# Kernel tuning notes

Hardware: AMD Instinct MI355X
Metric: run time of the kernel (lower is better)

The kernel has to match this reference:

```python
import jax, jax.numpy as jnp
import numpy as np

V, H, L, A, TH, B, T = 32000, 512, 4, 384, 2, 2, 32
FF = 4 * H


def _ln(x, w, b, eps=1e-5):
    m = x.mean(-1, keepdims=True)
    v = ((x - m) ** 2).mean(-1, keepdims=True)
    return (x - m) * jax.lax.rsqrt(v + eps) * w + b


def setup_inputs() -> dict:
    key = jax.random.key(0)
    ks = jax.random.split(key, 10)
    w = lambda k, shape, s=0.02: jax.random.normal(k, shape, jnp.float32) * s
    return {
        "input_ids": jax.random.randint(ks[0], (B, T), 0, V),
        "states": w(ks[1], (L, B, H, H), 0.1),
        "emb": w(ks[2], (V, H)),
        "nx_w": jnp.ones((L, H)), "nx_b": jnp.zeros((L, H)),
        "Wp": w(ks[3], (L, A + H, H)), "bp": jnp.zeros((L, A + H)),
        "Wg": w(ks[4], (L, H, H)), "Wt": w(ks[5], (L, H, H)),
        "ns_w": jnp.ones((L, H)), "ns_b": jnp.zeros((L, H)),
        "W1": w(ks[6], (L, FF, H)), "b1": jnp.zeros((L, FF)),
        "W2": w(ks[7], (L, H, FF)), "b2": jnp.zeros((L, H)),
        "on_w": jnp.ones((H,)), "on_b": jnp.zeros((H,)),
        "head_W": w(ks[8], (V, H)), "head_b": jnp.zeros((V,)),
    }


def _recur(lp, state, x):
    # state: [B,H,H]; x: [B,H]. Rank-1 low-rank update of the active rows,
    # gated tanh update of the ghost rows (Finch/Goose + GhostRNN).
    p = x @ lp["Wp"].T + lp["bp"]                  # [B, A+H]
    u, v = p[:, :A], p[:, A:]
    active_upd = u[:, :, None] * v[:, None, :]       # [B,A,H] = u @ v (rank 1)
    ghost = state[:, A:]                             # [B,H-A,H]
    gate = jax.nn.sigmoid(jnp.einsum('bgh,oh->bgo', ghost, lp["Wg"]))
    trans = jnp.tanh(jnp.einsum('bgh,oh->bgo', ghost, lp["Wt"]))
    return state + jnp.concatenate([active_upd, gate * trans], axis=1)


def _layer(lp, state, x):
    state = _recur(lp, state, _ln(x, lp["nx_w"], lp["nx_b"]))
    z = jnp.zeros_like(x)
    for _ in range(TH - 1):                          # latent "thinking" steps
        state = _recur(lp, state, z)
    x = x + state.mean(axis=1)                       # [B,H]
    h = _ln(x, lp["ns_w"], lp["ns_b"])
    h = jax.nn.gelu(h @ lp["W1"].T + lp["b1"], approximate=False)
    return state, x + h @ lp["W2"].T + lp["b2"]


def _forward(input_ids, states, emb, nx_w, nx_b, Wp, bp, Wg, Wt, ns_w, ns_b,
             W1, b1, W2, b2, on_w, on_b, head_W, head_b):
    lp = dict(nx_w=nx_w, nx_b=nx_b, Wp=Wp, bp=bp, Wg=Wg, Wt=Wt,
              ns_w=ns_w, ns_b=ns_b, W1=W1, b1=b1, W2=W2, b2=b2)
    x = jnp.swapaxes(emb[input_ids], 0, 1)           # [T,B,H]

    def step(st, tok):                               # scan over time
        def lstep(tok, inp):                         # scan over layers
            lpi, s = inp
            s, tok = _layer(lpi, s, tok)
            return tok, s
        tok, new_st = jax.lax.scan(lstep, tok, (lp, st))
        return new_st, tok

    fstates, outs = jax.lax.scan(step, states, x)    # outs: [T,B,H]
    y = _ln(jnp.swapaxes(outs, 0, 1), on_w, on_b)
    return y @ head_W.T + head_b, fstates


def reference(input_ids, states, emb, nx_w, nx_b, Wp, bp, Wg, Wt, ns_w, ns_b,
              W1, b1, W2, b2, on_w, on_b, head_W, head_b):
    return _forward(input_ids, states, emb, nx_w, nx_b, Wp, bp, Wg, Wt,
                    ns_w, ns_b, W1, b1, W2, b2, on_w, on_b, head_W, head_b)
```

## Files before the change

kernel.cpp:

```cpp
#include <hip/hip_runtime.h>
#include <hip/hip_bf16.h>
#include <math.h>
#include <stddef.h>

namespace {

constexpr int V = 32000, H = 512, L = 4, A = 384, B = 2, T = 32, FF = 2048;
constexpr long LOGITS = (long)B * T * V;
constexpr int GRID = 256, NT = 512;
constexpr int NXR = 32;
constexpr int NGB = 32;
constexpr float EPS = 1e-5f;

typedef short bf16x8 __attribute__((ext_vector_type(8)));
typedef float f32x4 __attribute__((ext_vector_type(4)));
typedef unsigned long long ull;
typedef unsigned long long ull2 __attribute__((ext_vector_type(2)));

struct WS {
  unsigned gbar_cnt, gbar_gen;
  unsigned pad0[62];
  unsigned p1c[L], p2c[L], p3c[L], grc[L];
  unsigned pad1[48];
  unsigned gcol_cnt2[L][T];
  unsigned gxcnt[L];
  unsigned gxcd[L][NGB];
  unsigned pad2[64];
  float gcol[L][T][B][H];
  float uv[T][L][B][A + H];
  float lnxs[T][L][B][H];
  float outs[T][B][H];
  float lnouts[T * B][H];
  float xn[3][T][B][H];
  float hbuf[L][2][B][FF];
  float initcol[L * B * H];
  float bus[4];
  float wU[L][H];
  uint4 bpk[L][2][2][16][32][64];
  ull afr[L][2][2][2][8][16][64][2];
};

union __align__(16) SMem {
  struct { unsigned xch[8][2][16][16]; float colp[8][2][16]; } gx;
  struct {
    unsigned wp[16][256];
    unsigned w1[64][256];
    unsigned w2[16][1024];
    float lnx[2][512];
    unsigned hb[2][1024];
    float xms[2][16];
    float2 red[8];
  } xp;
  struct { float u16[T][16]; float lnx[H]; } e1;
  struct { float tile[125][64]; } hd;
};

__device__ __forceinline__ float dot4(const float4& a, const float4& b) {
  return a.x * b.x + a.y * b.y + a.z * b.z + a.w * b.w;
}
__device__ __forceinline__ unsigned bf16r(float f) {
  unsigned u = __float_as_uint(f);
  return (u + 0x7fffu + ((u >> 16) & 1u)) >> 16;
}
__device__ __forceinline__ float sload(const float* p) {
  return __hip_atomic_load(p, __ATOMIC_RELAXED, __HIP_MEMORY_SCOPE_SYSTEM);
}
__device__ __forceinline__ void sstore(float* p, float v) {
  __hip_atomic_store(p, v, __ATOMIC_RELAXED, __HIP_MEMORY_SCOPE_SYSTEM);
}
__device__ __forceinline__ ull sld64(const ull* p) {
  return __hip_atomic_load(p, __ATOMIC_RELAXED, __HIP_MEMORY_SCOPE_SYSTEM);
}
__device__ __forceinline__ void sst64(ull* p, ull v) {
  __hip_atomic_store(p, v, __ATOMIC_RELAXED, __HIP_MEMORY_SCOPE_SYSTEM);
}
__device__ __forceinline__ ull ald64(const ull* p) {
  return __hip_atomic_load(p, __ATOMIC_RELAXED, __HIP_MEMORY_SCOPE_AGENT);
}
__device__ __forceinline__ void ast64(ull* p, ull v) {
  __hip_atomic_store(p, v, __ATOMIC_RELAXED, __HIP_MEMORY_SCOPE_AGENT);
}
__device__ __forceinline__ unsigned sload_u(const unsigned* p) {
  return __hip_atomic_load(p, __ATOMIC_RELAXED, __HIP_MEMORY_SCOPE_SYSTEM);
}
__device__ __forceinline__ f32x4 mfma16(bf16x8 a, bf16x8 b, f32x4 c) {
  return __builtin_amdgcn_mfma_f32_16x16x32_bf16(a, b, c, 0, 0, 0);
}
__device__ __forceinline__ bf16x8 bc2(ull a, ull b) {
  ull2 t; t.x = a; t.y = b;
  return __builtin_bit_cast(bf16x8, t);
}
__device__ __forceinline__ bf16x8 bcu4(uint4 u) {
  return __builtin_bit_cast(bf16x8, u);
}

template <bool FAST>
__device__ __forceinline__ bf16x8 ld_afr(const ull* p) {
  if (FAST) return bc2(ald64(p), ald64(p + 1));
  else      return bc2(sld64(p), sld64(p + 1));
}
template <bool FAST>
__device__ __forceinline__ void st_afr(ull* p, ull lo, ull hi) {
  if (FAST) { ast64(p, lo); ast64(p + 1, hi); }
  else      { sst64(p, lo); sst64(p + 1, hi); }
}

__device__ void wait_u32(unsigned* p, unsigned target) {
  int spin = 0;
  while (__hip_atomic_load(p, __ATOMIC_RELAXED, __HIP_MEMORY_SCOPE_AGENT) < target) {
    __builtin_amdgcn_s_sleep(8);
    if ((++spin & 63) == 0)
      (void)__hip_atomic_load(p, __ATOMIC_ACQUIRE, __HIP_MEMORY_SCOPE_AGENT);
  }
}

__device__ void gbar(WS* ws) {
  __syncthreads();
  if (threadIdx.x == 0) {
    __threadfence();
    unsigned g = __hip_atomic_load(&ws->gbar_gen, __ATOMIC_RELAXED, __HIP_MEMORY_SCOPE_AGENT);
    unsigned a = __hip_atomic_fetch_add(&ws->gbar_cnt, 1u, __ATOMIC_ACQ_REL, __HIP_MEMORY_SCOPE_AGENT);
    if (a == (unsigned)(GRID - 1)) {
      __hip_atomic_store(&ws->gbar_cnt, 0u, __ATOMIC_RELAXED, __HIP_MEMORY_SCOPE_AGENT);
      __hip_atomic_fetch_add(&ws->gbar_gen, 1u, __ATOMIC_RELEASE, __HIP_MEMORY_SCOPE_AGENT);
    } else {
      wait_u32(&ws->gbar_gen, g + 1);
    }
    __threadfence();
  }
  __syncthreads();
}

__device__ void cdone(unsigned* p) {
  __builtin_amdgcn_s_waitcnt(0);
  __syncthreads();
  if (threadIdx.x == 0)
    __hip_atomic_fetch_add(p, 1u, __ATOMIC_RELAXED, __HIP_MEMORY_SCOPE_AGENT);
}
__device__ void cwait(unsigned* p, unsigned tgt) {
  if (threadIdx.x == 0) {
    int spin = 0;
    while (sload_u(p) < tgt) {
      __builtin_amdgcn_s_sleep(2);
      if ((++spin & 1023) == 0)
        (void)__hip_atomic_load(p, __ATOMIC_ACQUIRE, __HIP_MEMORY_SCOPE_AGENT);
    }
  }
  __syncthreads();
}
__device__ void cwait2(unsigned* pa, unsigned ta, unsigned* pb, unsigned tbv) {
  if (threadIdx.x < 64) {
    unsigned* p = pa;
    unsigned tg = ta;
    if (threadIdx.x == 1) { p = pb; tg = tbv; }
    const bool act = threadIdx.x < 2;
    int spin = 0;
    for (;;) {
      bool ok = !act || sload_u(p) >= tg;
      if (__all(ok)) break;
      __builtin_amdgcn_s_sleep(2);
      if ((++spin & 1023) == 0 && act)
        (void)__hip_atomic_load(p, __ATOMIC_ACQUIRE, __HIP_MEMORY_SCOPE_AGENT);
    }
  }
  __syncthreads();
}

__device__ float2 wred2(float2 v) {
  #pragma unroll
  for (int off = 1; off < 64; off <<= 1) {
    v.x += __shfl_xor(v.x, off);
    v.y += __shfl_xor(v.y, off);
  }
  return v;
}

__device__ float2 block_red2(float2 v, SMem& sm) {
  v = wred2(v);
  int w = threadIdx.x >> 6;
  __syncthreads();
  if ((threadIdx.x & 63) == 0) sm.xp.red[w] = v;
  __syncthreads();
  float2 s{0.f, 0.f};
  #pragma unroll
  for (int q = 0; q < 8; ++q) { s.x += sm.xp.red[q].x; s.y += sm.xp.red[q].y; }
  return s;
}

__device__ void ln512(SMem& sm, const float* in, float* outp,
                      const float* w, const float* b) {
  int tid = threadIdx.x;
  float xv = in[tid];
  float m = block_red2({xv, 0.f}, sm).x * (1.f / H);
  float d = xv - m;
  float var = block_red2({d * d, 0.f}, sm).x * (1.f / H);
  float inv = rsqrtf(var + EPS);
  outp[tid] = d * inv * w[tid] + b[tid];
  __syncthreads();
}

__device__ float2 ln2reg(SMem& sm, float x0, float x1, const float* w, const float* b) {
  int tid = threadIdx.x;
  float2 mm = block_red2({x0, x1}, sm);
  float d0 = x0 - mm.x * (1.f / H), d1 = x1 - mm.y * (1.f / H);
  float2 vv = block_red2({d0 * d0, d1 * d1}, sm);
  float i0 = rsqrtf(vv.x * (1.f / H) + EPS), i1 = rsqrtf(vv.y * (1.f / H) + EPS);
  float wv_ = w[tid], bv = b[tid];
  float l0 = d0 * i0 * wv_ + bv, l1 = d1 * i1 * wv_ + bv;
  sm.xp.lnx[0][tid] = l0;
  sm.xp.lnx[1][tid] = l1;
  __syncthreads();
  return {l0, l1};
}

__device__ __forceinline__ float2 d8(uint4 wq, const float* xr0, const float* xr1) {
  float2 a{0.f, 0.f};
  unsigned u[4] = {wq.x, wq.y, wq.z, wq.w};
  #pragma unroll
  for (int j = 0; j < 4; ++j) {
    float wl = __uint_as_float(u[j] << 16);
    float wh = __uint_as_float(u[j] & 0xffff0000u);
    a.x = fmaf(wl, xr0[2 * j], fmaf(wh, xr0[2 * j + 1], a.x));
    a.y = fmaf(wl, xr1[2 * j], fmaf(wh, xr1[2 * j + 1], a.y));
  }
  return a;
}

template <bool FAST>
__device__ void ghost_regs(int l, int ct, WS* ws, SMem& sm,
                           const float* __restrict__ states, float* __restrict__ fs) {
  const int tid = threadIdx.x, wv = tid >> 6, lane = tid & 63;
  const int c15 = lane & 15, lq = lane >> 4;
  float ms[2][4];
  #pragma unroll
  for (int b = 0; b < 2; ++b)
    #pragma unroll
    for (int r = 0; r < 4; ++r)
      ms[b][r] = states[((((long)l * B + b) * H) + A + 16 * wv + 4 * lq + r) * H + 16 * ct + c15];

  const int ktp = ct >> 1;
  const int lt_base = 32 * (ct & 1);

  #pragma unroll 1
  for (int rec = 0; rec < 2 * T; ++rec) {
    const int pp = rec & 1, np = pp ^ 1;
    asm volatile("" ::: "memory");
    f32x4 accg[2], acct[2];
    #pragma unroll
    for (int b = 0; b < 2; ++b) { accg[b] = {0.f,0.f,0.f,0.f}; acct[b] = {0.f,0.f,0.f,0.f}; }
    #pragma unroll 4
    for (int kt = 0; kt < 16; ++kt) {
      bf16x8 a00 = ld_afr<FAST>(&ws->afr[l][pp][0][0][wv][kt][lane][0]);
      bf16x8 a01 = ld_afr<FAST>(&ws->afr[l][pp][0][1][wv][kt][lane][0]);
      bf16x8 a10 = ld_afr<FAST>(&ws->afr[l][pp][1][0][wv][kt][lane][0]);
      bf16x8 a11 = ld_afr<FAST>(&ws->afr[l][pp][1][1][wv][kt][lane][0]);
      bf16x8 bgh = bcu4(ws->bpk[l][0][0][kt][ct][lane]);
      bf16x8 bgl = bcu4(ws->bpk[l][0][1][kt][ct][lane]);
      bf16x8 bth = bcu4(ws->bpk[l][1][0][kt][ct][lane]);
      bf16x8 btl = bcu4(ws->bpk[l][1][1][kt][ct][lane]);
      accg[0] = mfma16(a00, bgh, accg[0]);
      accg[0] = mfma16(a00, bgl, accg[0]);
      accg[0] = mfma16(a01, bgh, accg[0]);
      acct[0] = mfma16(a00, bth, acct[0]);
      acct[0] = mfma16(a00, btl, acct[0]);
      acct[0] = mfma16(a01, bth, acct[0]);
      accg[1] = mfma16(a10, bgh, accg[1]);
      accg[1] = mfma16(a10, bgl, accg[1]);
      accg[1] = mfma16(a11, bgh, accg[1]);
      acct[1] = mfma16(a10, bth, acct[1]);
      acct[1] = mfma16(a10, btl, acct[1]);
      acct[1] = mfma16(a11, bth, acct[1]);
    }
    const int t = rec >> 1;
    const bool pub = (rec & 1) != 0;
    #pragma unroll
    for (int b = 0; b < 2; ++b) {
      float css = 0.f;
      #pragma unroll
      for (int r = 0; r < 4; ++r) {
        float sig = 1.f / (1.f + expf(-accg[b][r]));
        float nv = ms[b][r] + sig * tanhf(acct[b][r]);
        ms[b][r] = nv;
        css += nv;
        unsigned hi = bf16r(nv);
        unsigned lo = bf16r(nv - __uint_as_float(hi << 16));
        sm.gx.xch[wv][b][4 * lq + r][c15] = hi | (lo << 16);
      }
      if (pub) {
        css += __shfl_xor(css, 16);
        css += __shfl_xor(css, 32);
        if (lane < 16) sm.gx.colp[wv][b][lane] = css;
      }
    }
    __syncthreads();
    {
      const int b = lane >> 5, o2 = (lane >> 4) & 1, row = lane & 15;
      unsigned x[8];
      #pragma unroll
      for (int j = 0; j < 8; ++j) x[j] = sm.gx.xch[wv][b][row][o2 * 8 + j];
      unsigned hw[4], lw[4];
      #pragma unroll
      for (int j = 0; j < 4; ++j) {
        hw[j] = (x[2 * j] & 0xffffu) | ((x[2 * j + 1] & 0xffffu) << 16);
        lw[j] = (x[2 * j] >> 16) | (x[2 * j + 1] & 0xffff0000u);
      }
      const int lt = lt_base + 16 * o2 + row;
      st_afr<FAST>(&ws->afr[l][np][b][0][wv][ktp][lt][0],
                   hw[0] | ((ull)hw[1] << 32), hw[2] | ((ull)hw[3] << 32));
      st_afr<FAST>(&ws->afr[l][np][b][1][wv][ktp][lt][0],
                   lw[0] | ((ull)lw[1] << 32), lw[2] | ((ull)lw[3] << 32));
    }
    if (pub && tid < 32) {
      int b = tid >> 4, c = tid & 15;
      float s = 0.f;
      #pragma unroll
      for (int w = 0; w < 8; ++w) s += sm.gx.colp[w][b][c];
      sstore(&ws->gcol[l][t][b][16 * ct + c], s);
    }
    asm volatile("" ::: "memory");
    __builtin_amdgcn_s_waitcnt(0);
    __syncthreads();
    if (tid == 0) {
      __hip_atomic_fetch_add(&ws->grc[l], 1u, __ATOMIC_RELAXED, __HIP_MEMORY_SCOPE_AGENT);
      if (pub)
        __hip_atomic_fetch_add(&ws->gcol_cnt2[l][t], 1u, __ATOMIC_RELAXED, __HIP_MEMORY_SCOPE_AGENT);
    }
    if (rec + 1 < 2 * T) cwait(&ws->grc[l], (unsigned)(NGB * (rec + 1)));
  }
  #pragma unroll
  for (int b = 0; b < 2; ++b)
    #pragma unroll
    for (int r = 0; r < 4; ++r)
      fs[((((long)l * B + b) * H) + A + 16 * wv + 4 * lq + r) * H + 16 * ct + c15] = ms[b][r];
}

__device__ void x_set(int l, int role, WS* ws, SMem& sm,
                      const int* ids, const float* emb,
                      const float* nx_w, const float* nx_b,
                      const float* Wp, const float* bp,
                      const float* ns_w, const float* ns_b,
                      const float* W1, const float* b1,
                      const float* W2, const float* b2) {
  const int tid = threadIdx.x, wv = tid >> 6, lane = tid & 63;
  const long wb = (long)l * (A + H);
  const int v0r = role * 16, a0 = role * 64, c0 = role * 16;

  for (int i = tid; i < 16 * 256; i += NT) {
    int row = i >> 8, m = i & 255;
    const float* s = Wp + (wb + A + v0r + row) * H + 2 * m;
    sm.xp.wp[row][m] = bf16r(s[0]) | (bf16r(s[1]) << 16);
  }
  for (int i = tid; i < 64 * 256; i += NT) {
    int row = i >> 8, m = i & 255;
    const float* s = W1 + ((long)l * FF + a0 + row) * H + 2 * m;
    sm.xp.w1[row][m] = bf16r(s[0]) | (bf16r(s[1]) << 16);
  }
  for (int i = tid; i < 16 * 1024; i += NT) {
    int row = i >> 10, m = i & 1023;
    const float* s = W2 + ((long)l * H + c0 + row) * FF + 2 * m;
    sm.xp.w2[row][m] = bf16r(s[0]) | (bf16r(s[1]) << 16);
  }
  const float ic0 = ws->initcol[(l * B + 0) * H + tid];
  const float ic1 = ws->initcol[(l * B + 1) * H + tid];
  const float BU = ws->bus[l];
  const float bpA = bp[wb + A + tid];
  const float wU0 = ws->wU[l][tid];
  float as0 = 0.f, as1 = 0.f;
  __syncthreads();

  for (int t = 0; t < T; ++t) {
    float xm0, xm1;
    if (l == 0) {
      xm0 = emb[(long)ids[t] * H + tid];
      xm1 = emb[(long)ids[T + t] * H + tid];
    } else {
      cwait(&ws->p3c[l - 1], (unsigned)(NXR * (t + 1)));
      xm0 = sload(&ws->xn[l - 1][t][0][tid]);
      xm1 = sload(&ws->xn[l - 1][t][1][tid]);
    }
    float2 ln = ln2reg(sm, xm0, xm1, nx_w + l * H, nx_b + l * H);
    float xr0[8], xr1[8];
    #pragma unroll
    for (int j = 0; j < 8; ++j) { xr0[j] = sm.xp.lnx[0][lane * 8 + j]; xr1[j] = sm.xp.lnx[1][lane * 8 + j]; }
    #pragma unroll
    for (int it = 0; it < 2; ++it) {
      int row = v0r + wv + it * 8;
      uint4 wq = *(const uint4*)&sm.xp.wp[row - v0r][lane * 4];
      float2 acc = wred2(d8(wq, xr0, xr1));
      if (lane == 0) {
        float bb = bp[wb + A + row];
        sstore(&ws->uv[t][l][0][A + row], acc.x + bb);
        sstore(&ws->uv[t][l][1][A + row], acc.y + bb);
      }
    }
    if (tid >= v0r && tid < v0r + 16) {
      sstore(&ws->lnxs[t][l][0][tid], ln.x);
      sstore(&ws->lnxs[t][l][1][tid], ln.y);
    }
    cdone(&ws->p1c[l]);
    float2 U1 = block_red2({wU0 * ln.x, wU0 * ln.y}, sm);
    cwait2(&ws->p1c[l], (unsigned)(NXR * (t + 1)),
           &ws->gcol_cnt2[l][t], (unsigned)NGB);
    float v0 = sload(&ws->uv[t][l][0][A + tid]);
    float v1 = sload(&ws->uv[t][l][1][A + tid]);
    float gc0 = sload(&ws->gcol[l][t][0][tid]);
    float gc1 = sload(&ws->gcol[l][t][1][tid]);
    as0 += (U1.x + BU) * v0;
    as1 += (U1.y + BU) * v1;
    float tb = (float)(t + 1) * BU * bpA;
    xm0 += (as0 + ic0 + tb + gc0) * (1.f / H);
    xm1 += (as1 + ic1 + tb + gc1) * (1.f / H);
    if (tid >= c0 && tid < c0 + 16) { sm.xp.xms[0][tid - c0] = xm0; sm.xp.xms[1][tid - c0] = xm1; }
    ln = ln2reg(sm, xm0, xm1, ns_w + l * H, ns_b + l * H);
    #pragma unroll
    for (int j = 0; j < 8; ++j) { xr0[j] = sm.xp.lnx[0][lane * 8 + j]; xr1[j] = sm.xp.lnx[1][lane * 8 + j]; }
    #pragma unroll
    for (int it = 0; it < 8; ++it) {
      int row = a0 + wv + it * 8;
      uint4 wq = *(const uint4*)&sm.xp.w1[row - a0][lane * 4];
      float2 acc = wred2(d8(wq, xr0, xr1));
      if (lane == 0) {
        float bb = b1[(long)l * FF + row];
        float z0 = acc.x + bb, z1 = acc.y + bb;
        sstore(&ws->hbuf[l][t & 1][0][row], 0.5f * z0 * (1.f + erff(z0 * 0.70710678118f)));
        sstore(&ws->hbuf[l][t & 1][1][row], 0.5f * z1 * (1.f + erff(z1 * 0.70710678118f)));
      }
    }
    cdone(&ws->p2c[l]);
    cwait(&ws->p2c[l], (unsigned)(NXR * (t + 1)));
    for (int i = tid; i < 2048; i += NT) {
      int b = i >> 10, m = i & 1023;
      float h0 = sload(&ws->hbuf[l][t & 1][b][2 * m]);
      float h1 = sload(&ws->hbuf[l][t & 1][b][2 * m + 1]);
      sm.xp.hb[b][m] = bf16r(h0) | (bf16r(h1) << 16);
    }
    __syncthreads();
    unsigned h0r[16], h1r[16];
    #pragma unroll
    for (int q = 0; q < 16; ++q) { h0r[q] = sm.xp.hb[0][lane + 64 * q]; h1r[q] = sm.xp.hb[1][lane + 64 * q]; }
    #pragma unroll
    for (int it = 0; it < 2; ++it) {
      int row = c0 + wv + it * 8;
      float2 acc{0.f, 0.f};
      #pragma unroll
      for (int q = 0; q < 16; ++q) {
        unsigned w = sm.xp.w2[row - c0][lane + 64 * q];
        float wl = __uint_as_float(w << 16), wh = __uint_as_float(w & 0xffff0000u);
        acc.x += wl * __uint_as_float(h0r[q] << 16) + wh * __uint_as_float(h0r[q] & 0xffff0000u);
        acc.y += wl * __uint_as_float(h1r[q] << 16) + wh * __uint_as_float(h1r[q] & 0xffff0000u);
      }
      acc = wred2(acc);
      if (lane == 0) {
        float bb = b2[(long)l * H + row];
        float o0 = sm.xp.xms[0][row - c0] + acc.x + bb;
        float o1 = sm.xp.xms[1][row - c0] + acc.y + bb;
        if (l == L - 1) {
          sstore(&ws->outs[t][0][row], o0);
          sstore(&ws->outs[t][1][row], o1);
        } else {
          sstore(&ws->xn[l][t][0][row], o0);
          sstore(&ws->xn[l][t][1][row], o1);
        }
      }
    }
    cdone(&ws->p3c[l]);
  }
}

__global__ __launch_bounds__(256) void pack_kernel(const float* __restrict__ Wg,
                                                   const float* __restrict__ Wt,
                                                   const float* __restrict__ states,
                                                   const float* __restrict__ bp,
                                                   const float* __restrict__ Wp,
                                                   WS* ws) {
  const int bid = blockIdx.x, tid = threadIdx.x;
  if (bid < 1024) {
    #pragma unroll
    for (int rep = 0; rep < 2; ++rep) {
      unsigned f = (unsigned)bid * 512u + (unsigned)rep * 256u + (unsigned)tid;
      int lane = f & 63, ct = (f >> 6) & 31, kt = (f >> 11) & 15;
      int split = (f >> 15) & 1, mat = (f >> 16) & 1, l = f >> 17;
      int o = ct * 16 + (lane & 15), kb = kt * 32 + ((lane >> 4) << 3);
      const float* src = (mat ? Wt : Wg) + ((long)l * H + o) * H + kb;
      unsigned v8[8];
      #pragma unroll
      for (int j = 0; j < 8; ++j) {
        float w = src[j];
        unsigned h = bf16r(w);
        if (split) h = bf16r(w - __uint_as_float(h << 16));
        v8[j] = h;
      }
      uint4 u;
      u.x = v8[0] | (v8[1] << 16); u.y = v8[2] | (v8[3] << 16);
      u.z = v8[4] | (v8[5] << 16); u.w = v8[6] | (v8[7] << 16);
      ws->bpk[l][mat][split][kt][ct][lane] = u;
    }
  } else if (bid < 1032) {
    int lb = bid - 1024, l = lb >> 1, b = lb & 1;
    #pragma unroll
    for (int half = 0; half < 2; ++half) {
      int col = tid + half * 256;
      float acc = 0.f;
      for (int i = 0; i < A; ++i)
        acc += states[(((long)l * B + b) * H + i) * H + col];
      ws->initcol[(l * B + b) * H + col] = acc;
    }
  } else if (bid == 1032) {
    __shared__ float tmp[256];
    int l = tid >> 6, i = tid & 63;
    float p = 0.f;
    for (int j = 0; j < 6; ++j) p += bp[(long)l * (A + H) + j * 64 + i];
    tmp[tid] = p;
    __syncthreads();
    if (tid < 4) {
      float s = 0.f;
      for (int q = 0; q < 64; ++q) s += tmp[tid * 64 + q];
      ws->bus[tid] = s;
    }
  } else if (bid < 1037) {
    int l = bid - 1033;
    #pragma unroll
    for (int half = 0; half < 2; ++half) {
      int k = tid + half * 256;
      float acc = 0.f;
      for (int i = 0; i < A; ++i)
        acc += Wp[((long)l * (A + H) + i) * H + k];
      ws->wU[l][k] = acc;
    }
  } else {
    int q = bid - 1037, l = q >> 1, b = q & 1;
    for (int i = tid; i < 32768; i += 256) {
      int half = i & 1, lane = (i >> 1) & 63, kt = (i >> 7) & 15;
      int rt = (i >> 11) & 7, sp = (i >> 14) & 1;
      int g = 16 * rt + (lane & 15);
      int kb = 32 * kt + 8 * (lane >> 4) + 4 * half;
      const float* src = states + ((((long)l * B + b) * H) + A + g) * H + kb;
      unsigned v4[4];
      #pragma unroll
      for (int j = 0; j < 4; ++j) {
        float w = src[j];
        unsigned h = bf16r(w);
        if (sp) h = bf16r(w - __uint_as_float(h << 16));
        v4[j] = h;
      }
      unsigned w0 = v4[0] | (v4[1] << 16), w1 = v4[2] | (v4[3] << 16);
      ws->afr[l][0][b][sp][rt][kt][lane][half] = w0 | ((ull)w1 << 32);
    }
  }
}

__global__ __launch_bounds__(NT, 1) void vega_kernel(
    const int* __restrict__ ids, const float* __restrict__ states,
    const float* __restrict__ emb,
    const float* __restrict__ nx_w, const float* __restrict__ nx_b,
    const float* __restrict__ Wp, const float* __restrict__ bp,
    const float* __restrict__ ns_w, const float* __restrict__ ns_b,
    const float* __restrict__ W1, const float* __restrict__ b1,
    const float* __restrict__ W2, const float* __restrict__ b2,
    const float* __restrict__ on_w, const float* __restrict__ on_b,
    const float* __restrict__ head_W, const float* __restrict__ head_b,
    float* __restrict__ out, WS* ws) {
  __shared__ SMem sm;
  const int bid = blockIdx.x, tid = threadIdx.x;
  float* fs = out + LOGITS;

  const int c = bid & 7, j = bid >> 3;
  if (c < 4) {
    const int l = c, ct = j;
    unsigned myx = (unsigned)__builtin_amdgcn_s_getreg(6164);
    if (tid == 0) {
      __hip_atomic_store(&ws->gxcd[l][ct], myx | 0x100u,
                         __ATOMIC_RELAXED, __HIP_MEMORY_SCOPE_SYSTEM);
      __builtin_amdgcn_s_waitcnt(0);
      __hip_atomic_fetch_add(&ws->gxcnt[l], 1u, __ATOMIC_RELAXED, __HIP_MEMORY_SCOPE_AGENT);
    }
    cwait(&ws->gxcnt[l], (unsigned)NGB);
    unsigned x0 = sload_u(&ws->gxcd[l][0]);
    bool fast = true;
    for (int i = 1; i < NGB; ++i) fast = fast && (sload_u(&ws->gxcd[l][i]) == x0);
    if (fast) ghost_regs<true>(l, ct, ws, sm, states, fs);
    else      ghost_regs<false>(l, ct, ws, sm, states, fs);
  } else {
    x_set(c - 4, j, ws, sm, ids, emb, nx_w, nx_b, Wp, bp,
          ns_w, ns_b, W1, b1, W2, b2);
  }

  gbar(ws);

  if (bid < 192) {
    int lb = bid / 24, sub = bid % 24;
    int l = lb >> 1, b = lb & 1, r0 = sub * 16;
    const long wb = (long)l * (A + H);
    const int row = tid >> 5, kc = tid & 31;
    float wreg[16];
    {
      const float* wr = Wp + (wb + r0 + row) * H + kc * 16;
      #pragma unroll
      for (int jj = 0; jj < 16; ++jj) wreg[jj] = wr[jj];
    }
    const float bprow = bp[wb + r0 + row];
    float pre = sload(&ws->lnxs[0][l][b][tid]);
    for (int t2 = 0; t2 < T; ++t2) {
      sm.e1.lnx[tid] = pre;
      __syncthreads();
      if (t2 + 1 < T) pre = sload(&ws->lnxs[t2 + 1][l][b][tid]);
      float part = 0.f;
      #pragma unroll
      for (int jj = 0; jj < 16; ++jj) part += wreg[jj] * sm.e1.lnx[kc * 16 + jj];
      #pragma unroll
      for (int off = 1; off < 32; off <<= 1) part += __shfl_xor(part, off);
      if (kc == 0) sm.e1.u16[t2][row] = part + bprow;
      __syncthreads();
    }
    float bv = bp[wb + A + tid];
    float acc[16];
    #pragma unroll
    for (int q = 0; q < 16; ++q) acc[q] = 32.f * bp[wb + r0 + q] * bv;
    for (int t2 = 0; t2 < T; ++t2) {
      float vv = sload(&ws->uv[t2][l][b][A + tid]);
      #pragma unroll
      for (int q = 0; q < 16; ++q) acc[q] = fmaf(sm.e1.u16[t2][q], vv, acc[q]);
    }
    #pragma unroll
    for (int q = 0; q < 16; ++q)
      fs[(((long)l * B + b) * H + (r0 + q)) * H + tid] =
          states[(((long)l * B + b) * H + (r0 + q)) * H + tid] + acc[q];
  }
  if (bid < T * B) {
    int row = bid, t = row >> 1, b = row & 1;
    ln512(sm, ws->outs[t][b], ws->lnouts[row], on_w, on_b);
  }

  gbar(ws);

  {
    const int wv = tid >> 6, lane = tid & 63;
    const long vbase = (long)bid * 125;
    float acc[16];
    #pragma unroll
    for (int q = 0; q < 16; ++q) acc[q] = 0.f;
    for (int cc = 0; cc < 8; ++cc) {
      float4 xr[16];
      #pragma unroll
      for (int q = 0; q < 16; ++q)
        xr[q] = *(const float4*)&ws->lnouts[lane][cc * 64 + q * 4];
      #pragma unroll
      for (int vi = 0; vi < 16; ++vi) {
        int vloc = vi * 8 + wv;
        if (vloc < 125) {
          const float4* wp_ = (const float4*)(head_W + (vbase + vloc) * H + cc * 64);
          float s = 0.f;
          #pragma unroll
          for (int q = 0; q < 16; ++q) s += dot4(xr[q], wp_[q]);
          acc[vi] += s;
        }
      }
    }
    #pragma unroll
    for (int vi = 0; vi < 16; ++vi) {
      int vloc = vi * 8 + wv;
      if (vloc < 125) sm.hd.tile[vloc][lane] = acc[vi] + head_b[vbase + vloc];
    }
    __syncthreads();
    for (int idx = tid; idx < 64 * 125; idx += NT) {
      int row = idx / 125, vl = idx % 125;
      int t = row >> 1, b = row & 1;
      out[((long)(b * T + t)) * V + vbase + vl] = sm.hd.tile[vl][row];
    }
  }
}

}

extern "C" void kernel_launch(void* const* d_in, const int* in_sizes, int n_in,
                              void* d_out, int out_size, void* d_ws, size_t ws_size,
                              hipStream_t stream) {
  (void)in_sizes; (void)n_in; (void)out_size; (void)ws_size;
  const int*   ids    = (const int*)d_in[0];
  const float* states = (const float*)d_in[1];
  const float* emb    = (const float*)d_in[2];
  const float* nx_w   = (const float*)d_in[3];
  const float* nx_b   = (const float*)d_in[4];
  const float* Wp     = (const float*)d_in[5];
  const float* bp     = (const float*)d_in[6];
  const float* Wg     = (const float*)d_in[7];
  const float* Wt     = (const float*)d_in[8];
  const float* ns_w   = (const float*)d_in[9];
  const float* ns_b   = (const float*)d_in[10];
  const float* W1     = (const float*)d_in[11];
  const float* b1     = (const float*)d_in[12];
  const float* W2     = (const float*)d_in[13];
  const float* b2     = (const float*)d_in[14];
  const float* on_w   = (const float*)d_in[15];
  const float* on_b   = (const float*)d_in[16];
  const float* head_W = (const float*)d_in[17];
  const float* head_b = (const float*)d_in[18];
  float* out = (float*)d_out;
  WS* ws = (WS*)d_ws;

  (void)hipMemsetAsync(d_ws, 0, offsetof(WS, uv), stream);
  pack_kernel<<<dim3(1045), dim3(256), 0, stream>>>(Wg, Wt, states, bp, Wp, ws);
  vega_kernel<<<dim3(GRID), dim3(NT), 0, stream>>>(
      ids, states, emb, nx_w, nx_b, Wp, bp, ns_w, ns_b,
      W1, b1, W2, b2, on_w, on_b, head_W, head_b, out, ws);
}
```

Measured before the change: 1.640 ms.

## Replace atomic counters with per-block flag arrays and polled barriers

Replaces the fetch-add counters used for cross-block phase signalling and the global barrier with one flag word per producer block, written with plain system-scope stores and polled by a wavefront that checks all 32 (or 256) flags at once. Barrier release becomes a single master block that gathers the flags and publishes a release word. The aim is to remove serialized atomic RMW contention and lower the latency of the many per-timestep handoffs in this persistent kernel. It also loads the hbuf pairs as 64-bit values. In exchange it adds more polling traffic, and correctness now depends on the flags being monotone and on the workspace starting zeroed.

```diff
diff --git a/kernel.cpp b/kernel.cpp
--- a/kernel.cpp
+++ b/kernel.cpp
@@ -18,12 +18,12 @@
 typedef unsigned long long ull2 __attribute__((ext_vector_type(2)));
 
 struct WS {
-  unsigned gbar_cnt, gbar_gen;
-  unsigned pad0[62];
-  unsigned p1c[L], p2c[L], p3c[L], grc[L];
-  unsigned pad1[48];
-  unsigned gcol_cnt2[L][T];
-  unsigned gxcnt[L];
+  unsigned gflag[GRID];
+  unsigned grel;
+  unsigned pad0[63];
+  unsigned p1f[L][NXR], p2f[L][NXR], p3f[L][NXR];
+  unsigned gbf[L][NGB];
+  unsigned gcf[L][T][NGB];
   unsigned gxcd[L][NGB];
   unsigned pad2[64];
   float gcol[L][T][B][H];
@@ -83,6 +83,9 @@
 __device__ __forceinline__ unsigned sload_u(const unsigned* p) {
   return __hip_atomic_load(p, __ATOMIC_RELAXED, __HIP_MEMORY_SCOPE_SYSTEM);
 }
+__device__ __forceinline__ void sstore_u(unsigned* p, unsigned v) {
+  __hip_atomic_store(p, v, __ATOMIC_RELAXED, __HIP_MEMORY_SCOPE_SYSTEM);
+}
 __device__ __forceinline__ f32x4 mfma16(bf16x8 a, bf16x8 b, f32x4 c) {
   return __builtin_amdgcn_mfma_f32_16x16x32_bf16(a, b, c, 0, 0, 0);
 }
@@ -105,63 +108,62 @@
   else      { sst64(p, lo); sst64(p + 1, hi); }
 }
 
-__device__ void wait_u32(unsigned* p, unsigned target) {
-  int spin = 0;
-  while (__hip_atomic_load(p, __ATOMIC_RELAXED, __HIP_MEMORY_SCOPE_AGENT) < target) {
-    __builtin_amdgcn_s_sleep(8);
-    if ((++spin & 63) == 0)
-      (void)__hip_atomic_load(p, __ATOMIC_ACQUIRE, __HIP_MEMORY_SCOPE_AGENT);
-  }
-}
-
-__device__ void gbar(WS* ws) {
+__device__ void poll32(const unsigned* f, unsigned tgt) {
+  if (threadIdx.x < 64) {
+    const bool act = threadIdx.x < 32;
+    const unsigned* p = f + (act ? threadIdx.x : 0);
+    for (;;) {
+      unsigned v = sload_u(p);
+      if (__all(!act || v >= tgt)) break;
+      __builtin_amdgcn_s_sleep(1);
+    }
+  }
+  __syncthreads();
+}
+__device__ void poll_dual(const unsigned* fa, unsigned ta,
+                          const unsigned* fb, unsigned tb) {
+  if (threadIdx.x < 64) {
+    const bool ina = threadIdx.x < 32;
+    const unsigned* p = ina ? fa + threadIdx.x : fb + (threadIdx.x - 32);
+    const unsigned tg = ina ? ta : tb;
+    for (;;) {
+      unsigned v = sload_u(p);
+      if (__all(v >= tg)) break;
+      __builtin_amdgcn_s_sleep(1);
+    }
+  }
+  __syncthreads();
+}
+__device__ void setf_sys(unsigned* p, unsigned v) {
+  __builtin_amdgcn_s_waitcnt(0);
+  __syncthreads();
+  if (threadIdx.x == 0) sstore_u(p, v);
+}
+
+__device__ void gbar2(WS* ws, unsigned phase) {
+  __builtin_amdgcn_s_waitcnt(0);
   __syncthreads();
   if (threadIdx.x == 0) {
     __threadfence();
-    unsigned g = __hip_atomic_load(&ws->gbar_gen, __ATOMIC_RELAXED, __HIP_MEMORY_SCOPE_AGENT);
-    unsigned a = __hip_atomic_fetch_add(&ws->gbar_cnt, 1u, __ATOMIC_ACQ_REL, __HIP_MEMORY_SCOPE_AGENT);
-    if (a == (unsigned)(GRID - 1)) {
-      __hip_atomic_store(&ws->gbar_cnt, 0u, __ATOMIC_RELAXED, __HIP_MEMORY_SCOPE_AGENT);
-      __hip_atomic_fetch_add(&ws->gbar_gen, 1u, __ATOMIC_RELEASE, __HIP_MEMORY_SCOPE_AGENT);
-    } else {
-      wait_u32(&ws->gbar_gen, g + 1);
-    }
+    sstore_u(&ws->gflag[blockIdx.x], phase);
+  }
+  if (blockIdx.x == 0) {
+    if (threadIdx.x < 64) {
+      for (;;) {
+        bool ok = true;
+        #pragma unroll
+        for (int q = 0; q < 4; ++q)
+          ok = ok && (sload_u(&ws->gflag[threadIdx.x * 4 + q]) >= phase);
+        if (__all(ok)) break;
+        __builtin_amdgcn_s_sleep(1);
+      }
+    }
+    __syncthreads();
+    if (threadIdx.x == 0) sstore_u(&ws->grel, phase);
+  }
+  if (threadIdx.x == 0) {
+    while (sload_u(&ws->grel) < phase) __builtin_amdgcn_s_sleep(1);
     __threadfence();
-  }
-  __syncthreads();
-}
-
-__device__ void cdone(unsigned* p) {
-  __builtin_amdgcn_s_waitcnt(0);
-  __syncthreads();
-  if (threadIdx.x == 0)
-    __hip_atomic_fetch_add(p, 1u, __ATOMIC_RELAXED, __HIP_MEMORY_SCOPE_AGENT);
-}
-__device__ void cwait(unsigned* p, unsigned tgt) {
-  if (threadIdx.x == 0) {
-    int spin = 0;
-    while (sload_u(p) < tgt) {
-      __builtin_amdgcn_s_sleep(2);
-      if ((++spin & 1023) == 0)
-        (void)__hip_atomic_load(p, __ATOMIC_ACQUIRE, __HIP_MEMORY_SCOPE_AGENT);
-    }
-  }
-  __syncthreads();
-}
-__device__ void cwait2(unsigned* pa, unsigned ta, unsigned* pb, unsigned tbv) {
-  if (threadIdx.x < 64) {
-    unsigned* p = pa;
-    unsigned tg = ta;
-    if (threadIdx.x == 1) { p = pb; tg = tbv; }
-    const bool act = threadIdx.x < 2;
-    int spin = 0;
-    for (;;) {
-      bool ok = !act || sload_u(p) >= tg;
-      if (__all(ok)) break;
-      __builtin_amdgcn_s_sleep(2);
-      if ((++spin & 1023) == 0 && act)
-        (void)__hip_atomic_load(p, __ATOMIC_ACQUIRE, __HIP_MEMORY_SCOPE_AGENT);
-    }
   }
   __syncthreads();
 }
@@ -321,11 +323,10 @@
     __builtin_amdgcn_s_waitcnt(0);
     __syncthreads();
     if (tid == 0) {
-      __hip_atomic_fetch_add(&ws->grc[l], 1u, __ATOMIC_RELAXED, __HIP_MEMORY_SCOPE_AGENT);
-      if (pub)
-        __hip_atomic_fetch_add(&ws->gcol_cnt2[l][t], 1u, __ATOMIC_RELAXED, __HIP_MEMORY_SCOPE_AGENT);
-    }
-    if (rec + 1 < 2 * T) cwait(&ws->grc[l], (unsigned)(NGB * (rec + 1)));
+      sstore_u(&ws->gbf[l][ct], (unsigned)(rec + 1));
+      if (pub) sstore_u(&ws->gcf[l][t][ct], 1u);
+    }
+    if (rec + 1 < 2 * T) poll32(ws->gbf[l], (unsigned)(rec + 1));
   }
   #pragma unroll
   for (int b = 0; b < 2; ++b)
@@ -374,7 +375,7 @@
       xm0 = emb[(long)ids[t] * H + tid];
       xm1 = emb[(long)ids[T + t] * H + tid];
     } else {
-      cwait(&ws->p3c[l - 1], (unsigned)(NXR * (t + 1)));
+      poll32(ws->p3f[l - 1], (unsigned)(t + 1));
       xm0 = sload(&ws->xn[l - 1][t][0][tid]);
       xm1 = sload(&ws->xn[l - 1][t][1][tid]);
     }
@@ -397,10 +398,9 @@
       sstore(&ws->lnxs[t][l][0][tid], ln.x);
       sstore(&ws->lnxs[t][l][1][tid], ln.y);
     }
-    cdone(&ws->p1c[l]);
+    setf_sys(&ws->p1f[l][role], (unsigned)(t + 1));
     float2 U1 = block_red2({wU0 * ln.x, wU0 * ln.y}, sm);
-    cwait2(&ws->p1c[l], (unsigned)(NXR * (t + 1)),
-           &ws->gcol_cnt2[l][t], (unsigned)NGB);
+    poll_dual(ws->p1f[l], (unsigned)(t + 1), ws->gcf[l][t], 1u);
     float v0 = sload(&ws->uv[t][l][0][A + tid]);
     float v1 = sload(&ws->uv[t][l][1][A + tid]);
     float gc0 = sload(&ws->gcol[l][t][0][tid]);
@@ -426,12 +426,13 @@
         sstore(&ws->hbuf[l][t & 1][1][row], 0.5f * z1 * (1.f + erff(z1 * 0.70710678118f)));
       }
     }
-    cdone(&ws->p2c[l]);
-    cwait(&ws->p2c[l], (unsigned)(NXR * (t + 1)));
+    setf_sys(&ws->p2f[l][role], (unsigned)(t + 1));
+    poll32(ws->p2f[l], (unsigned)(t + 1));
     for (int i = tid; i < 2048; i += NT) {
       int b = i >> 10, m = i & 1023;
-      float h0 = sload(&ws->hbuf[l][t & 1][b][2 * m]);
-      float h1 = sload(&ws->hbuf[l][t & 1][b][2 * m + 1]);
+      ull hv = sld64((const ull*)&ws->hbuf[l][t & 1][b][2 * m]);
+      float h0 = __uint_as_float((unsigned)hv);
+      float h1 = __uint_as_float((unsigned)(hv >> 32));
       sm.xp.hb[b][m] = bf16r(h0) | (bf16r(h1) << 16);
     }
     __syncthreads();
@@ -463,7 +464,8 @@
         }
       }
     }
-    cdone(&ws->p3c[l]);
+    setf_sys(&ws->p3f[l][role], (unsigned)(t + 1));
+    __syncthreads();
   }
 }
 
@@ -568,13 +570,8 @@
   if (c < 4) {
     const int l = c, ct = j;
     unsigned myx = (unsigned)__builtin_amdgcn_s_getreg(6164);
-    if (tid == 0) {
-      __hip_atomic_store(&ws->gxcd[l][ct], myx | 0x100u,
-                         __ATOMIC_RELAXED, __HIP_MEMORY_SCOPE_SYSTEM);
-      __builtin_amdgcn_s_waitcnt(0);
-      __hip_atomic_fetch_add(&ws->gxcnt[l], 1u, __ATOMIC_RELAXED, __HIP_MEMORY_SCOPE_AGENT);
-    }
-    cwait(&ws->gxcnt[l], (unsigned)NGB);
+    if (tid == 0) sstore_u(&ws->gxcd[l][ct], myx | 0x100u);
+    poll32(ws->gxcd[l], 0x100u);
     unsigned x0 = sload_u(&ws->gxcd[l][0]);
     bool fast = true;
     for (int i = 1; i < NGB; ++i) fast = fast && (sload_u(&ws->gxcd[l][i]) == x0);
@@ -585,7 +582,7 @@
           ns_w, ns_b, W1, b1, W2, b2);
   }
 
-  gbar(ws);
+  gbar2(ws, 1u);
 
   if (bid < 192) {
     int lb = bid / 24, sub = bid % 24;
@@ -631,7 +628,7 @@
     ln512(sm, ws->outs[t][b], ws->lnouts[row], on_w, on_b);
   }
 
-  gbar(ws);
+  gbar2(ws, 2u);
 
   {
     const int wv = tid >> 6, lane = tid & 63;
```

New measurement: 1.535 ms. 6.4% less time.
